# Kernel tuning notes

Hardware: AMD Instinct MI355X
Metric: run time of the kernel (lower is better)

## Reference

```python
import jax, jax.numpy as jnp
import numpy as np

N, OUT, IN = 16384, 2048, 2048

def setup_inputs() -> dict:
    key = jax.random.key(0)
    k1, k2, k3 = jax.random.split(key, 3)
    input_ = jax.random.normal(k1, (N, IN), dtype=jnp.float32)
    # kaiming normal, fan_in mode: std = sqrt(2/fan_in)
    weight = jax.random.normal(k2, (OUT, IN), dtype=jnp.float32) * np.sqrt(2.0 / IN)
    mask = jax.random.randint(k3, (OUT, IN), 0, 2, dtype=jnp.int32)
    return {"input_": input_, "weight": weight, "mask": mask}

def reference(input_, weight, mask):
    # out = x @ (W * mask)^T  -- mask is a fixed binary expander pattern
    masked_w = weight * mask.astype(weight.dtype)  # [OUT, IN]
    return jnp.matmul(input_, masked_w.T)          # [N, OUT]
```

## Files before the change

### kernel.cpp

```cpp
#include <hip/hip_runtime.h>


#define MDIM 16384
#define NDIM 2048
#define KDIM 2048

#define BM 256
#define BN 128
#define GRID_X ((MDIM / BM) * (NDIM / BN))

using f32x4   = __attribute__((ext_vector_type(4))) float;
using bf16x8  = __attribute__((ext_vector_type(8))) __bf16;
using ushort8 = __attribute__((ext_vector_type(8))) unsigned short;

typedef __attribute__((address_space(3))) const unsigned short* lds_cptr_t;

__device__ __forceinline__ unsigned short f2bf(float f) {
  unsigned int u = __builtin_bit_cast(unsigned int, f);
  u = u + 0x7FFFu + ((u >> 16) & 1u);
  return (unsigned short)(u >> 16);
}


__global__ void convert_input_kernel(const float* __restrict__ in,
                                     unsigned short* __restrict__ out) {
  size_t base = ((size_t)blockIdx.x * blockDim.x + threadIdx.x) * 8;
  float4 a = *reinterpret_cast<const float4*>(in + base);
  float4 b = *reinterpret_cast<const float4*>(in + base + 4);
  ushort8 v;
  v[0] = f2bf(a.x); v[1] = f2bf(a.y); v[2] = f2bf(a.z); v[3] = f2bf(a.w);
  v[4] = f2bf(b.x); v[5] = f2bf(b.y); v[6] = f2bf(b.z); v[7] = f2bf(b.w);
  *reinterpret_cast<ushort8*>(out + base) = v;
}

__global__ void convert_weight_kernel(const float* __restrict__ w,
                                      const int* __restrict__ mk,
                                      unsigned short* __restrict__ out) {
  size_t base = ((size_t)blockIdx.x * blockDim.x + threadIdx.x) * 8;
  float4 a = *reinterpret_cast<const float4*>(w + base);
  float4 b = *reinterpret_cast<const float4*>(w + base + 4);
  int4 m0 = *reinterpret_cast<const int4*>(mk + base);
  int4 m1 = *reinterpret_cast<const int4*>(mk + base + 4);
  ushort8 v;
  v[0] = m0.x ? f2bf(a.x) : (unsigned short)0;
  v[1] = m0.y ? f2bf(a.y) : (unsigned short)0;
  v[2] = m0.z ? f2bf(a.z) : (unsigned short)0;
  v[3] = m0.w ? f2bf(a.w) : (unsigned short)0;
  v[4] = m1.x ? f2bf(b.x) : (unsigned short)0;
  v[5] = m1.y ? f2bf(b.y) : (unsigned short)0;
  v[6] = m1.z ? f2bf(b.z) : (unsigned short)0;
  v[7] = m1.w ? f2bf(b.w) : (unsigned short)0;
  *reinterpret_cast<ushort8*>(out + base) = v;
}


__device__ __forceinline__ f32x4 MF(bf16x8 a, bf16x8 b, f32x4 c) {
  return __builtin_amdgcn_mfma_f32_16x16x32_bf16(a, b, c, 0, 0, 0);
}
#define VMCNT(n) asm volatile("s_waitcnt vmcnt(" #n ")" ::: "memory")
#define LGKM(n)  asm volatile("s_waitcnt lgkmcnt(" #n ")" ::: "memory")
#define DSR(dst, p, off)                                                        \
  asm volatile("ds_read_b128 %0, %1 offset:%2" : "=v"(dst) : "v"(p), "i"(off))

__global__ __launch_bounds__(256, 2) void gemm_occ2(
    const unsigned short* __restrict__ Abf,
    const unsigned short* __restrict__ Bbf,
    float* __restrict__ C) {
  __shared__ __attribute__((aligned(16))) unsigned short Asl[2 * 8192];
  __shared__ __attribute__((aligned(16))) unsigned short Bsl[2 * 4096];

  int bid = blockIdx.x;
  int wgs = (bid & 7) * (GRID_X / 8) + (bid >> 3);
  int tm = wgs >> 4;
  int tn = wgs & 15;
  int row0 = tm * BM, col0 = tn * BN;

  int t = threadIdx.x;
  int lane = t & 63, wid = t >> 6;
  int wr = wid >> 1, wc = wid & 1;
  int fr = lane & 15, fq = lane >> 4;

  int p0 = wid * 64 + lane;
  int r0 = p0 >> 2, kc0 = ((p0 & 3) ^ ((r0 >> 1) & 3)) * 8;
  size_t offA0 = (size_t)(row0 + r0) * KDIM + kc0;
  size_t offB0 = (size_t)(col0 + r0) * KDIM + kc0;
  int ldsw = wid * 512;

  int kxor = (fq ^ ((fr >> 1) & 3)) * 8;
  int aoff = (wr * 128 + fr) * 32 + kxor;
  int boff = (wc * 64 + fr) * 32 + kxor;
  lds_cptr_t aA = ((lds_cptr_t)Asl) + aoff;
  lds_cptr_t aB = ((lds_cptr_t)Bsl) + boff;

  f32x4 acc[8][4];
#pragma unroll
  for (int m = 0; m < 8; ++m)
#pragma unroll
    for (int n = 0; n < 4; ++n) acc[m][n] = f32x4{0.f, 0.f, 0.f, 0.f};

  bf16x8 aP[8], bP[4], aQ[8], bQ[4];

#define STGA(sa, ke) do {                                                       \
  _Pragma("unroll")                                                             \
  for (int _j = 0; _j < 4; ++_j)                                                \
    __builtin_amdgcn_global_load_lds(                                           \
        (const __attribute__((address_space(1))) void*)(Abf + offA0 +           \
                                                        _j * 131072 + (ke)),    \
        (__attribute__((address_space(3))) void*)(Asl + (sa) * 8192 +           \
                                                  _j * 2048 + ldsw),            \
        16, 0, 0);                                                              \
} while (0)
#define STGB(sb, ke) do {                                                       \
  _Pragma("unroll")                                                             \
  for (int _j = 0; _j < 2; ++_j)                                                \
    __builtin_amdgcn_global_load_lds(                                           \
        (const __attribute__((address_space(1))) void*)(Bbf + offB0 +           \
                                                        _j * 131072 + (ke)),    \
        (__attribute__((address_space(3))) void*)(Bsl + (sb) * 4096 +           \
                                                  _j * 2048 + ldsw),            \
        16, 0, 0);                                                              \
} while (0)

#define RD12(s, AD, BD) do {                                                    \
  DSR(AD[0], aA, (s) * 16384 + 0 * 1024);                                       \
  DSR(BD[0], aB, (s) * 8192 + 0 * 1024);                                        \
  DSR(BD[1], aB, (s) * 8192 + 1 * 1024);                                        \
  DSR(BD[2], aB, (s) * 8192 + 2 * 1024);                                        \
  DSR(BD[3], aB, (s) * 8192 + 3 * 1024);                                        \
  DSR(AD[1], aA, (s) * 16384 + 1 * 1024);                                       \
  DSR(AD[2], aA, (s) * 16384 + 2 * 1024);                                       \
  DSR(AD[3], aA, (s) * 16384 + 3 * 1024);                                       \
  DSR(AD[4], aA, (s) * 16384 + 4 * 1024);                                       \
  DSR(AD[5], aA, (s) * 16384 + 5 * 1024);                                       \
  DSR(AD[6], aA, (s) * 16384 + 6 * 1024);                                       \
  DSR(AD[7], aA, (s) * 16384 + 7 * 1024);                                       \
} while (0)

#define PHASE(rs, AC, BC, AD, BD, STAGES) do {                                  \
  VMCNT(0);                                                                     \
  LGKM(0);                                                                      \
  __builtin_amdgcn_s_barrier();                                                 \
  __builtin_amdgcn_sched_barrier(0);                                            \
  STAGES;                                                                       \
  __builtin_amdgcn_sched_barrier(0);                                            \
  __builtin_amdgcn_s_setprio(1);                                                \
  _Pragma("unroll")                                                             \
  for (int _m = 0; _m < 4; ++_m)                                                \
    _Pragma("unroll")                                                           \
    for (int _n = 0; _n < 4; ++_n)                                              \
      acc[_m][_n] = MF(AC[_m], BC[_n], acc[_m][_n]);                            \
  RD12(rs, AD, BD);                                                             \
  _Pragma("unroll")                                                             \
  for (int _m = 4; _m < 8; ++_m)                                                \
    _Pragma("unroll")                                                           \
    for (int _n = 0; _n < 4; ++_n)                                              \
      acc[_m][_n] = MF(AC[_m], BC[_n], acc[_m][_n]);                            \
  __builtin_amdgcn_s_setprio(0);                                                \
} while (0)

  STGA(0, 0);  STGB(0, 0);
  STGA(1, 32); STGB(1, 32);
  VMCNT(6);
  __builtin_amdgcn_s_barrier();
  RD12(0, aP, bP);

  for (int i = 0; i < 31; ++i) {
    int kb = i * 64;
    PHASE(1, aP, bP, aQ, bQ, { STGA(0, kb + 64); STGB(0, kb + 64); });
    PHASE(0, aQ, bQ, aP, bP, { STGA(1, kb + 96); STGB(1, kb + 96); });
  }
  PHASE(1, aP, bP, aQ, bQ, );
  {
    LGKM(0);
    __builtin_amdgcn_sched_barrier(0);
#pragma unroll
    for (int m = 0; m < 8; ++m)
#pragma unroll
      for (int n = 0; n < 4; ++n)
        acc[m][n] = MF(aQ[m], bQ[n], acc[m][n]);
  }

  size_t crow = (size_t)(row0 + wr * 128 + fq * 4);
  int ccol = col0 + wc * 64 + fr;
#pragma unroll
  for (int m = 0; m < 8; ++m)
#pragma unroll
    for (int n = 0; n < 4; ++n) {
      float* cp = C + (crow + m * 16) * NDIM + ccol + n * 16;
#pragma unroll
      for (int e = 0; e < 4; ++e) cp[(size_t)e * NDIM] = acc[m][n][e];
    }
#undef PHASE
#undef RD12
#undef STGA
#undef STGB
}


__global__ __launch_bounds__(256) void gemm_fused_fallback(
    const float* __restrict__ Afp,
    const float* __restrict__ Wfp,
    const int* __restrict__ Mk,
    float* __restrict__ C) {
  __shared__ unsigned short As[128 * 32];
  __shared__ unsigned short Bs[128 * 32];
  int bid = blockIdx.x;
  int nwg = (MDIM / 128) * (NDIM / 128);
  int wg = (bid & 7) * (nwg / 8) + (bid >> 3);
  int tm = wg >> 4, tn = wg & 15;
  int row0 = tm * 128, col0 = tn * 128;
  int t = threadIdx.x;
  int lane = t & 63, wv = t >> 6;
  int wr = wv >> 1, wc = wv & 1;
  int fr = lane & 15, fq = lane >> 4;
  f32x4 acc[4][4];
#pragma unroll
  for (int i = 0; i < 4; ++i)
#pragma unroll
    for (int j = 0; j < 4; ++j) acc[i][j] = f32x4{0.f, 0.f, 0.f, 0.f};
  for (int kt = 0; kt < KDIM; kt += 32) {
#pragma unroll
    for (int j = 0; j < 2; ++j) {
      int c = j * 256 + t;
      int r = c >> 2;
      int ko = (c & 3) * 8;
      const float* ga = Afp + (size_t)(row0 + r) * KDIM + kt + ko;
      float4 a0 = *reinterpret_cast<const float4*>(ga);
      float4 a1 = *reinterpret_cast<const float4*>(ga + 4);
      ushort8 va;
      va[0] = f2bf(a0.x); va[1] = f2bf(a0.y); va[2] = f2bf(a0.z); va[3] = f2bf(a0.w);
      va[4] = f2bf(a1.x); va[5] = f2bf(a1.y); va[6] = f2bf(a1.z); va[7] = f2bf(a1.w);
      *reinterpret_cast<ushort8*>(As + (size_t)c * 8) = va;
      const float* gw = Wfp + (size_t)(col0 + r) * KDIM + kt + ko;
      const int* gm = Mk + (size_t)(col0 + r) * KDIM + kt + ko;
      float4 w0 = *reinterpret_cast<const float4*>(gw);
      float4 w1 = *reinterpret_cast<const float4*>(gw + 4);
      int4 m0 = *reinterpret_cast<const int4*>(gm);
      int4 m1 = *reinterpret_cast<const int4*>(gm + 4);
      ushort8 vb;
      vb[0] = m0.x ? f2bf(w0.x) : (unsigned short)0;
      vb[1] = m0.y ? f2bf(w0.y) : (unsigned short)0;
      vb[2] = m0.z ? f2bf(w0.z) : (unsigned short)0;
      vb[3] = m0.w ? f2bf(w0.w) : (unsigned short)0;
      vb[4] = m1.x ? f2bf(w1.x) : (unsigned short)0;
      vb[5] = m1.y ? f2bf(w1.y) : (unsigned short)0;
      vb[6] = m1.z ? f2bf(w1.z) : (unsigned short)0;
      vb[7] = m1.w ? f2bf(w1.w) : (unsigned short)0;
      *reinterpret_cast<ushort8*>(Bs + (size_t)c * 8) = vb;
    }
    __syncthreads();
    bf16x8 af[4], bfr[4];
#pragma unroll
    for (int m2 = 0; m2 < 4; ++m2)
      af[m2] = *reinterpret_cast<const bf16x8*>(As + (wr * 64 + m2 * 16 + fr) * 32 + fq * 8);
#pragma unroll
    for (int n2 = 0; n2 < 4; ++n2)
      bfr[n2] = *reinterpret_cast<const bf16x8*>(Bs + (wc * 64 + n2 * 16 + fr) * 32 + fq * 8);
#pragma unroll
    for (int m2 = 0; m2 < 4; ++m2)
#pragma unroll
      for (int n2 = 0; n2 < 4; ++n2)
        acc[m2][n2] = MF(af[m2], bfr[n2], acc[m2][n2]);
    __syncthreads();
  }
#pragma unroll
  for (int m2 = 0; m2 < 4; ++m2)
#pragma unroll
    for (int n2 = 0; n2 < 4; ++n2) {
      size_t r0 = (size_t)(row0 + wr * 64 + m2 * 16 + fq * 4);
      size_t c0 = (size_t)(col0 + wc * 64 + n2 * 16 + fr);
#pragma unroll
      for (int i = 0; i < 4; ++i) C[(r0 + i) * NDIM + c0] = acc[m2][n2][i];
    }
}


extern "C" void kernel_launch(void* const* d_in, const int* in_sizes, int n_in,
                              void* d_out, int out_size, void* d_ws, size_t ws_size,
                              hipStream_t stream) {
  const float* input  = (const float*)d_in[0];
  const float* weight = (const float*)d_in[1];
  const int*   mask   = (const int*)d_in[2];
  float* out = (float*)d_out;

  const size_t needA = (size_t)MDIM * KDIM * sizeof(unsigned short);
  const size_t needB = (size_t)NDIM * KDIM * sizeof(unsigned short);

  if (ws_size >= needA + needB) {
    unsigned short* Abf = (unsigned short*)d_ws;
    unsigned short* Bbf = (unsigned short*)((char*)d_ws + needA);
    convert_input_kernel<<<(MDIM * (size_t)KDIM / 8) / 256, 256, 0, stream>>>(input, Abf);
    convert_weight_kernel<<<(NDIM * (size_t)KDIM / 8) / 256, 256, 0, stream>>>(weight, mask, Bbf);
    gemm_occ2<<<GRID_X, 256, 0, stream>>>(Abf, Bbf, out);
  } else {
    int nwg = (MDIM / 128) * (NDIM / 128);
    gemm_fused_fallback<<<nwg, 256, 0, stream>>>(input, weight, mask, out);
  }
}
```

Baseline: 183.3 us.

## Fuse fp32-to-bf16 input conversion into GEMM with 256x256 tiles and triple buffering

Removes the separate input conversion kernel and its bf16 workspace round-trip. The GEMM now loads fp32 activations into registers, converts them to bf16 and writes them to LDS itself. The tile grows to 256x256 with 512 threads and three LDS stages so register-staged A loads can overlap compute. In exchange, A is read as fp32 (twice the bytes) and conversion ALU work sits inside the main loop. LDS and register pressure also rise, which may cost occupancy.

```diff
diff --git a/kernel.cpp b/kernel.cpp
--- a/kernel.cpp
+++ b/kernel.cpp
@@ -6,7 +6,7 @@
 #define KDIM 2048
 
 #define BM 256
-#define BN 128
+#define BN 256
 #define GRID_X ((MDIM / BM) * (NDIM / BN))
 
 using f32x4   = __attribute__((ext_vector_type(4))) float;
@@ -21,17 +21,6 @@
   return (unsigned short)(u >> 16);
 }
 
-
-__global__ void convert_input_kernel(const float* __restrict__ in,
-                                     unsigned short* __restrict__ out) {
-  size_t base = ((size_t)blockIdx.x * blockDim.x + threadIdx.x) * 8;
-  float4 a = *reinterpret_cast<const float4*>(in + base);
-  float4 b = *reinterpret_cast<const float4*>(in + base + 4);
-  ushort8 v;
-  v[0] = f2bf(a.x); v[1] = f2bf(a.y); v[2] = f2bf(a.z); v[3] = f2bf(a.w);
-  v[4] = f2bf(b.x); v[5] = f2bf(b.y); v[6] = f2bf(b.z); v[7] = f2bf(b.w);
-  *reinterpret_cast<ushort8*>(out + base) = v;
-}
 
 __global__ void convert_weight_kernel(const float* __restrict__ w,
                                       const int* __restrict__ mk,
@@ -62,29 +51,30 @@
 #define DSR(dst, p, off)                                                        \
   asm volatile("ds_read_b128 %0, %1 offset:%2" : "=v"(dst) : "v"(p), "i"(off))
 
-__global__ __launch_bounds__(256, 2) void gemm_occ2(
-    const unsigned short* __restrict__ Abf,
+__global__ __launch_bounds__(512, 2) void gemm_fc(
+    const float* __restrict__ Afp,
     const unsigned short* __restrict__ Bbf,
     float* __restrict__ C) {
-  __shared__ __attribute__((aligned(16))) unsigned short Asl[2 * 8192];
-  __shared__ __attribute__((aligned(16))) unsigned short Bsl[2 * 4096];
+  __shared__ __attribute__((aligned(16))) unsigned short Asl[3 * 8192];
+  __shared__ __attribute__((aligned(16))) unsigned short Bsl[3 * 8192];
 
   int bid = blockIdx.x;
   int wgs = (bid & 7) * (GRID_X / 8) + (bid >> 3);
-  int tm = wgs >> 4;
-  int tn = wgs & 15;
+  int tm = wgs >> 3;
+  int tn = wgs & 7;
   int row0 = tm * BM, col0 = tn * BN;
 
   int t = threadIdx.x;
   int lane = t & 63, wid = t >> 6;
-  int wr = wid >> 1, wc = wid & 1;
+  int wr = wid >> 2, wc = wid & 3;
   int fr = lane & 15, fq = lane >> 4;
 
-  int p0 = wid * 64 + lane;
+  int p0 = (wid * 2) * 64 + lane;
   int r0 = p0 >> 2, kc0 = ((p0 & 3) ^ ((r0 >> 1) & 3)) * 8;
-  size_t offA0 = (size_t)(row0 + r0) * KDIM + kc0;
+  size_t offAf = (size_t)(row0 + r0) * KDIM + kc0;
   size_t offB0 = (size_t)(col0 + r0) * KDIM + kc0;
-  int ldsw = wid * 512;
+  int ldsw0 = (wid * 2) * 512;
+  int wbA = ldsw0 + lane * 8;
 
   int kxor = (fq ^ ((fr >> 1) & 3)) * 8;
   int aoff = (wr * 128 + fr) * 32 + kxor;
@@ -99,34 +89,44 @@
     for (int n = 0; n < 4; ++n) acc[m][n] = f32x4{0.f, 0.f, 0.f, 0.f};
 
   bf16x8 aP[8], bP[4], aQ[8], bQ[4];
-
-#define STGA(sa, ke) do {                                                       \
-  _Pragma("unroll")                                                             \
-  for (int _j = 0; _j < 4; ++_j)                                                \
-    __builtin_amdgcn_global_load_lds(                                           \
-        (const __attribute__((address_space(1))) void*)(Abf + offA0 +           \
-                                                        _j * 131072 + (ke)),    \
-        (__attribute__((address_space(3))) void*)(Asl + (sa) * 8192 +           \
-                                                  _j * 2048 + ldsw),            \
-        16, 0, 0);                                                              \
-} while (0)
+  float4 aU[4], aV[4];
+
+#define ALD(S, ke) do {                                                         \
+  S[0] = *reinterpret_cast<const float4*>(Afp + offAf + (ke));                  \
+  S[1] = *reinterpret_cast<const float4*>(Afp + offAf + (ke) + 4);              \
+  S[2] = *reinterpret_cast<const float4*>(Afp + offAf + 32768 + (ke));          \
+  S[3] = *reinterpret_cast<const float4*>(Afp + offAf + 32768 + (ke) + 4);      \
+} while (0)
+
+#define CONV(sw, S) do {                                                        \
+  ushort8 _w;                                                                   \
+  _w[0] = f2bf(S[0].x); _w[1] = f2bf(S[0].y);                                   \
+  _w[2] = f2bf(S[0].z); _w[3] = f2bf(S[0].w);                                   \
+  _w[4] = f2bf(S[1].x); _w[5] = f2bf(S[1].y);                                   \
+  _w[6] = f2bf(S[1].z); _w[7] = f2bf(S[1].w);                                   \
+  *reinterpret_cast<ushort8*>(Asl + (sw) * 8192 + wbA) = _w;                    \
+  _w[0] = f2bf(S[2].x); _w[1] = f2bf(S[2].y);                                   \
+  _w[2] = f2bf(S[2].z); _w[3] = f2bf(S[2].w);                                   \
+  _w[4] = f2bf(S[3].x); _w[5] = f2bf(S[3].y);                                   \
+  _w[6] = f2bf(S[3].z); _w[7] = f2bf(S[3].w);                                   \
+  *reinterpret_cast<ushort8*>(Asl + (sw) * 8192 + wbA + 512) = _w;              \
+} while (0)
+
 #define STGB(sb, ke) do {                                                       \
-  _Pragma("unroll")                                                             \
-  for (int _j = 0; _j < 2; ++_j)                                                \
-    __builtin_amdgcn_global_load_lds(                                           \
-        (const __attribute__((address_space(1))) void*)(Bbf + offB0 +           \
-                                                        _j * 131072 + (ke)),    \
-        (__attribute__((address_space(3))) void*)(Bsl + (sb) * 4096 +           \
-                                                  _j * 2048 + ldsw),            \
-        16, 0, 0);                                                              \
+  __builtin_amdgcn_global_load_lds(                                             \
+      (const __attribute__((address_space(1))) void*)(Bbf + offB0 + (ke)),      \
+      (__attribute__((address_space(3))) void*)(Bsl + (sb) * 8192 + ldsw0),     \
+      16, 0, 0);                                                                \
+  __builtin_amdgcn_global_load_lds(                                             \
+      (const __attribute__((address_space(1))) void*)(Bbf + offB0 + 32768 +     \
+                                                      (ke)),                    \
+      (__attribute__((address_space(3))) void*)(Bsl + (sb) * 8192 + ldsw0 +     \
+                                                512),                           \
+      16, 0, 0);                                                                \
 } while (0)
 
 #define RD12(s, AD, BD) do {                                                    \
   DSR(AD[0], aA, (s) * 16384 + 0 * 1024);                                       \
-  DSR(BD[0], aB, (s) * 8192 + 0 * 1024);                                        \
-  DSR(BD[1], aB, (s) * 8192 + 1 * 1024);                                        \
-  DSR(BD[2], aB, (s) * 8192 + 2 * 1024);                                        \
-  DSR(BD[3], aB, (s) * 8192 + 3 * 1024);                                        \
   DSR(AD[1], aA, (s) * 16384 + 1 * 1024);                                       \
   DSR(AD[2], aA, (s) * 16384 + 2 * 1024);                                       \
   DSR(AD[3], aA, (s) * 16384 + 3 * 1024);                                       \
@@ -134,10 +134,14 @@
   DSR(AD[5], aA, (s) * 16384 + 5 * 1024);                                       \
   DSR(AD[6], aA, (s) * 16384 + 6 * 1024);                                       \
   DSR(AD[7], aA, (s) * 16384 + 7 * 1024);                                       \
-} while (0)
-
-#define PHASE(rs, AC, BC, AD, BD, STAGES) do {                                  \
-  VMCNT(0);                                                                     \
+  DSR(BD[0], aB, (s) * 16384 + 0 * 1024);                                       \
+  DSR(BD[1], aB, (s) * 16384 + 1 * 1024);                                       \
+  DSR(BD[2], aB, (s) * 16384 + 2 * 1024);                                       \
+  DSR(BD[3], aB, (s) * 16384 + 3 * 1024);                                       \
+} while (0)
+
+#define PH(AC, BC, AD, BD, snb, STAGES, CONVBLK, WAITS) do {                    \
+  WAITS;                                                                        \
   LGKM(0);                                                                      \
   __builtin_amdgcn_s_barrier();                                                 \
   __builtin_amdgcn_sched_barrier(0);                                            \
@@ -149,7 +153,8 @@
     _Pragma("unroll")                                                           \
     for (int _n = 0; _n < 4; ++_n)                                              \
       acc[_m][_n] = MF(AC[_m], BC[_n], acc[_m][_n]);                            \
-  RD12(rs, AD, BD);                                                             \
+  CONVBLK;                                                                      \
+  RD12(snb, AD, BD);                                                            \
   _Pragma("unroll")                                                             \
   for (int _m = 4; _m < 8; ++_m)                                                \
     _Pragma("unroll")                                                           \
@@ -158,18 +163,36 @@
   __builtin_amdgcn_s_setprio(0);                                                \
 } while (0)
 
-  STGA(0, 0);  STGB(0, 0);
-  STGA(1, 32); STGB(1, 32);
-  VMCNT(6);
+  ALD(aU, 0);  STGB(0, 0);
+  VMCNT(2);
+  CONV(0, aU);
+  ALD(aV, 32); STGB(1, 32);
+  VMCNT(2);
+  CONV(1, aV);
+  ALD(aU, 64); STGB(2, 64);
+  LGKM(0);
   __builtin_amdgcn_s_barrier();
   RD12(0, aP, bP);
 
-  for (int i = 0; i < 31; ++i) {
-    int kb = i * 64;
-    PHASE(1, aP, bP, aQ, bQ, { STGA(0, kb + 64); STGB(0, kb + 64); });
-    PHASE(0, aQ, bQ, aP, bP, { STGA(1, kb + 96); STGB(1, kb + 96); });
+  for (int i = 0; i < 10; ++i) {
+    int kb = i * 192;
+    PH(aP, bP, aQ, bQ, 1, { ALD(aV, kb +  96); STGB(0, kb +  96); },
+       CONV(2, aU), VMCNT(2));
+    PH(aQ, bQ, aP, bP, 2, { ALD(aU, kb + 128); STGB(1, kb + 128); },
+       CONV(0, aV), VMCNT(2));
+    PH(aP, bP, aQ, bQ, 0, { ALD(aV, kb + 160); STGB(2, kb + 160); },
+       CONV(1, aU), VMCNT(2));
+    PH(aQ, bQ, aP, bP, 1, { ALD(aU, kb + 192); STGB(0, kb + 192); },
+       CONV(2, aV), VMCNT(2));
+    PH(aP, bP, aQ, bQ, 2, { ALD(aV, kb + 224); STGB(1, kb + 224); },
+       CONV(0, aU), VMCNT(2));
+    PH(aQ, bQ, aP, bP, 0, { ALD(aU, kb + 256); STGB(2, kb + 256); },
+       CONV(1, aV), VMCNT(2));
   }
-  PHASE(1, aP, bP, aQ, bQ, );
+  PH(aP, bP, aQ, bQ, 1, { ALD(aV, 2016); STGB(0, 2016); },
+     CONV(2, aU), VMCNT(2));
+  PH(aQ, bQ, aP, bP, 2, , CONV(0, aV), VMCNT(2));
+  PH(aP, bP, aQ, bQ, 0, , , VMCNT(0));
   {
     LGKM(0);
     __builtin_amdgcn_sched_barrier(0);
@@ -190,10 +213,11 @@
 #pragma unroll
       for (int e = 0; e < 4; ++e) cp[(size_t)e * NDIM] = acc[m][n][e];
     }
-#undef PHASE
+#undef PH
 #undef RD12
-#undef STGA
 #undef STGB
+#undef CONV
+#undef ALD
 }
 
 
@@ -283,15 +307,12 @@
   const int*   mask   = (const int*)d_in[2];
   float* out = (float*)d_out;
 
-  const size_t needA = (size_t)MDIM * KDIM * sizeof(unsigned short);
   const size_t needB = (size_t)NDIM * KDIM * sizeof(unsigned short);
 
-  if (ws_size >= needA + needB) {
-    unsigned short* Abf = (unsigned short*)d_ws;
-    unsigned short* Bbf = (unsigned short*)((char*)d_ws + needA);
-    convert_input_kernel<<<(MDIM * (size_t)KDIM / 8) / 256, 256, 0, stream>>>(input, Abf);
+  if (ws_size >= needB) {
+    unsigned short* Bbf = (unsigned short*)d_ws;
     convert_weight_kernel<<<(NDIM * (size_t)KDIM / 8) / 256, 256, 0, stream>>>(weight, mask, Bbf);
-    gemm_occ2<<<GRID_X, 256, 0, stream>>>(Abf, Bbf, out);
+    gemm_fc<<<GRID_X, 512, 0, stream>>>(input, Bbf, out);
   } else {
     int nwg = (MDIM / 128) * (NDIM / 128);
     gemm_fused_fallback<<<nwg, 256, 0, stream>>>(input, weight, mask, out);
```

Measured after the change: 244.2 us. 1.33x slower.
